# Kernel tuning notes

Hardware: AMD Instinct MI355X
Metric: run time of the kernel (lower is better)

## Reference

```python
import jax, jax.numpy as jnp
import numpy as np
from jax import lax

B, C, H, W = 16, 128, 128, 128
COUT, KH, KW, K, RED, TEMP = 128, 3, 3, 4, 4, 30.0
ATTN_CH = max(C // RED, 1)

def setup_inputs() -> dict:
    key = jax.random.key(0)
    ks = jax.random.split(key, 7)
    fan_out = COUT * KH * KW
    std = np.sqrt(2.0 / fan_out)  # kaiming_normal fan_out, relu
    return {
        "x": jax.random.normal(ks[0], (B, C, H, W), dtype=jnp.float32),
        "weight": jax.random.normal(ks[1], (K, COUT, C, KH, KW), dtype=jnp.float32) * std,
        "bias": jnp.zeros((K, COUT), dtype=jnp.float32),
        "aw1": jax.random.normal(ks[2], (ATTN_CH, C), dtype=jnp.float32) * (1.0 / np.sqrt(C)),
        "ab1": jnp.zeros((ATTN_CH,), dtype=jnp.float32),
        "aw2": jax.random.normal(ks[3], (K, ATTN_CH), dtype=jnp.float32) * (1.0 / np.sqrt(ATTN_CH)),
        "ab2": jnp.zeros((K,), dtype=jnp.float32),
    }

def reference(x, weight, bias, aw1, ab1, aw2, ab2):
    # Attention branch: global avg pool -> 1x1 conv -> relu -> 1x1 conv
    pooled = jnp.mean(x, axis=(2, 3))                       # (B, C)
    h = jax.nn.relu(pooled @ aw1.T + ab1)                   # (B, attn_ch)
    scores = h @ aw2.T + ab2                                # (B, K)
    attn = jax.nn.softmax(scores / TEMP, axis=1)            # (B, K)

    # Per-sample aggregated kernel and bias
    agg_w = jnp.einsum('bk,koipq->boipq', attn, weight)     # (B, Cout, Cin, kH, kW)
    agg_b = attn @ bias                                     # (B, Cout)

    # Per-sample conv2d (stride 1, padding 1, dilation 1, groups 1)
    def conv_one(xi, wi):
        return lax.conv_general_dilated(
            xi[None], wi,
            window_strides=(1, 1),
            padding=((1, 1), (1, 1)),
            dimension_numbers=('NCHW', 'OIHW', 'NCHW'),
        )[0]

    out = jax.vmap(conv_one)(x, agg_w)                      # (B, Cout, H, W)
    return out + agg_b[:, :, None, None]
```

## Files before the change

kernel.cpp:

```cpp
#include <hip/hip_runtime.h>

typedef float f32x4 __attribute__((ext_vector_type(4)));
typedef short bf16x8 __attribute__((ext_vector_type(8)));

__device__ __forceinline__ unsigned short f2bf(float f) {
  unsigned u = __builtin_bit_cast(unsigned, f);
  u = (u + 0x7FFFu + ((u >> 16) & 1u)) >> 16;
  return (unsigned short)u;
}

__device__ __forceinline__ void async16(const unsigned short* g, unsigned short* l) {
  __builtin_amdgcn_global_load_lds(
      (__attribute__((address_space(1))) void*)g,
      (__attribute__((address_space(3))) void*)l, 16, 0, 0);
}

#define XT_ROW 16640

__global__ __launch_bounds__(256) void k_transpose(const float* __restrict__ x,
                                                   unsigned short* __restrict__ xt,
                                                   float* __restrict__ rowsum) {
  __shared__ unsigned short tile[128][128];
  __shared__ float psum[128][8];
  const int y = blockIdx.x, b = blockIdx.y;
  const int t = threadIdx.x;
  const int colb = (t & 7) * 16;
  const int cp = t >> 3;
  const int swz = (t & 7) << 3;
  for (int ci = 0; ci < 4; ++ci) {
    const int c = ci * 32 + cp;
    const int c2 = c ^ swz;
    const float* src = x + (((size_t)(b * 128 + c) * 128 + y) * 128 + colb);
    float s = 0.f;
#pragma unroll
    for (int j = 0; j < 16; j += 4) {
      float4 v = *(const float4*)(src + j);
      s += v.x + v.y + v.z + v.w;
      tile[colb + j + 0][c2] = f2bf(v.x);
      tile[colb + j + 1][c2] = f2bf(v.y);
      tile[colb + j + 2][c2] = f2bf(v.z);
      tile[colb + j + 3][c2] = f2bf(v.w);
    }
    psum[c][t & 7] = s;
  }
  __syncthreads();
#pragma unroll
  for (int it = 0; it < 8; ++it) {
    const int slot = t + it * 256;
    const int col = slot >> 4;
    const int cg = (slot & 15) * 8;
    const int c2 = cg ^ (((col >> 4) & 7) << 3);
    uint4 vv = *(const uint4*)&tile[col][c2];
    *(uint4*)(xt + (((size_t)b * 130 + y + 1) * 130 + col + 1) * 128 + cg) = vv;
  }
  if (t < 128) {
    float r = 0.f;
#pragma unroll
    for (int j = 0; j < 8; ++j) r += psum[t][j];
    rowsum[((size_t)b * 128 + t) * 128 + y] = r;
  }
}

__global__ __launch_bounds__(256) void k_border(unsigned short* __restrict__ xt) {
  const int b = blockIdx.y;
  const int idx = blockIdx.x * 256 + threadIdx.x;
  if (idx >= 8256) return;
  int row, col, ck;
  if (idx < 4160) {
    row = (idx < 2080) ? 0 : 129;
    const int s = idx % 2080;
    col = s >> 4;
    ck = s & 15;
  } else {
    const int s = idx - 4160;
    row = (s >> 5) + 1;
    col = (s & 16) ? 129 : 0;
    ck = s & 15;
  }
  uint4 z = {0, 0, 0, 0};
  *(uint4*)(xt + ((size_t)b * 130 + row) * 130 * 128 + (size_t)col * 128 + ck * 8) = z;
}

__global__ __launch_bounds__(128) void k_attn(const float* __restrict__ rowsum,
                                              const float* __restrict__ aw1,
                                              const float* __restrict__ ab1,
                                              const float* __restrict__ aw2,
                                              const float* __restrict__ ab2,
                                              const float* __restrict__ bias,
                                              float* __restrict__ attn,
                                              float* __restrict__ aggb) {
  __shared__ float pooled[128];
  __shared__ float h[32];
  __shared__ float at[4];
  const int b = blockIdx.x, t = threadIdx.x;
  const float* rs = rowsum + (size_t)(b * 128 + t) * 128;
  float s = 0.f;
  for (int yy = 0; yy < 128; ++yy) s += rs[yy];
  pooled[t] = s * (1.f / 16384.f);
  __syncthreads();
  if (t < 32) {
    float hv = ab1[t];
    for (int c = 0; c < 128; ++c) hv += pooled[c] * aw1[t * 128 + c];
    h[t] = fmaxf(hv, 0.f);
  }
  __syncthreads();
  if (t < 4) {
    float sc = ab2[t];
    for (int a = 0; a < 32; ++a) sc += h[a] * aw2[t * 32 + a];
    at[t] = sc * (1.f / 30.f);
  }
  __syncthreads();
  if (t == 0) {
    float m = fmaxf(fmaxf(at[0], at[1]), fmaxf(at[2], at[3]));
    float e0 = __expf(at[0] - m), e1 = __expf(at[1] - m);
    float e2 = __expf(at[2] - m), e3 = __expf(at[3] - m);
    float inv = 1.f / (e0 + e1 + e2 + e3);
    at[0] = e0 * inv; at[1] = e1 * inv; at[2] = e2 * inv; at[3] = e3 * inv;
  }
  __syncthreads();
  if (t < 4) attn[b * 4 + t] = at[t];
  float ab = 0.f;
  for (int k = 0; k < 4; ++k) ab += at[k] * bias[k * 128 + t];
  aggb[b * 128 + t] = ab;
}

__global__ __launch_bounds__(256) void k_aggw(const float* __restrict__ weight,
                                              const float* __restrict__ attn,
                                              unsigned short* __restrict__ aggw) {
  const int fid = blockIdx.x * 256 + threadIdx.x;
  const int kk = fid & 31;
  const int o = (fid >> 5) & 127;
  const int rest = fid >> 12;
  const int s = rest % 36;
  const int b = rest / 36;
  const int c = ((s & 3) << 5) + kk;
  const int pq = s >> 2;
  const size_t src = (size_t)o * 1152 + (size_t)c * 9 + pq;
  float v = attn[b * 4 + 0] * weight[src]
          + attn[b * 4 + 1] * weight[src + 147456]
          + attn[b * 4 + 2] * weight[src + 2 * 147456]
          + attn[b * 4 + 3] * weight[src + 3 * 147456];
  aggw[fid] = f2bf(v);
}

__global__ __launch_bounds__(512, 1) void k_conv(const unsigned short* __restrict__ xt,
                                                 const unsigned short* __restrict__ aggw,
                                                 const float* __restrict__ aggb,
                                                 float* __restrict__ out) {
  __shared__ unsigned short lds[81920];
  const int id = blockIdx.x;
  const int swz = (id & 7) * 128 + (id >> 3);
  const int b = swz >> 6;
  const int y0 = (swz & 63) * 2;
  const int t = threadIdx.x;
  const int lane = t & 63, w = t >> 6;
  const int mw = w >> 2, nw = w & 3;
  const int l15 = lane & 15, lk = lane >> 4;

  {
    const unsigned short* xb = xt + (size_t)(b * 130 + y0) * XT_ROW;
#pragma unroll
    for (int i = 0; i < 16; ++i) {
      const int idx = i * 512 + t;
      const int row = idx >> 11, col = (idx >> 4) & 127, k8 = idx & 15;
      async16(xb + (row * 130 + col + 1) * 128 + ((k8 ^ (col & 15)) * 8),
              &lds[0] + i * 4096 + w * 512);
    }
  }
  const int an = t >> 2, ak8 = t & 3;
  const unsigned short* aS = aggw + (size_t)b * 147456 + an * 32
                           + ((ak8 ^ ((an >> 1) & 3)) * 8);
  unsigned short* aldsw = &lds[65536] + w * 512;

#define STAGE_A(buf, s) async16(aS + (s) * 4096, aldsw + (buf) * 4096)

  STAGE_A(0, 0);
  STAGE_A(1, 1);

  const int r_ = nw >> 1;
  const int px0 = (nw & 1) * 64 + l15;
  f32x4 acc[4][4] = {};

#pragma unroll
  for (int g = 0; g < 18; ++g) {
    asm volatile("s_waitcnt vmcnt(0)" ::: "memory");
    __builtin_amdgcn_sched_barrier(0);
    __builtin_amdgcn_s_barrier();
    __builtin_amdgcn_sched_barrier(0);
    if (g + 1 < 18) { STAGE_A((2 * g + 2) & 3, 2 * g + 2);
                      STAGE_A((2 * g + 3) & 3, 2 * g + 3); }
    __builtin_amdgcn_sched_barrier(0);
#pragma unroll
    for (int ss = 0; ss < 2; ++ss) {
      const int s = 2 * g + ss;
      const int tap = s >> 2, cc = s & 3;
      const int p = tap / 3, q = tap - 3 * p;
      const unsigned short* A0 = &lds[65536 + (s & 3) * 4096];
      bf16x8 af[4], bfr[4];
#pragma unroll
      for (int mi = 0; mi < 4; ++mi) {
        const int row = mw * 64 + mi * 16 + l15;
        af[mi] = *(const bf16x8*)(A0 + row * 32 + ((lk ^ ((row >> 1) & 3)) * 8));
      }
#pragma unroll
      for (int ni = 0; ni < 4; ++ni) {
        const int icol = px0 + ni * 16 + q - 1;
        int ccl = icol;
        if (q == 0 && ni == 0) ccl = (icol < 0) ? 0 : icol;
        if (q == 2 && ni == 3) ccl = (icol > 127) ? 127 : icol;
        bfr[ni] = *(const bf16x8*)(&lds[0] + ((r_ + p) * 128 + ccl) * 128
                                   + (((cc * 4 + lk) ^ (ccl & 15)) * 8));
        if (q == 0 && ni == 0) { if (icol < 0)   bfr[ni] = (bf16x8)0; }
        if (q == 2 && ni == 3) { if (icol > 127) bfr[ni] = (bf16x8)0; }
      }
      __builtin_amdgcn_s_setprio(1);
#pragma unroll
      for (int mi = 0; mi < 4; ++mi)
#pragma unroll
        for (int ni = 0; ni < 4; ++ni)
          acc[mi][ni] = __builtin_amdgcn_mfma_f32_16x16x32_bf16(af[mi], bfr[ni], acc[mi][ni], 0, 0, 0);
      __builtin_amdgcn_s_setprio(0);
    }
  }
#undef STAGE_A

  const int y = y0 + r_;
  const int colb = (nw & 1) * 64 + l15;
#pragma unroll
  for (int mi = 0; mi < 4; ++mi) {
    const int o = mw * 64 + mi * 16 + lk * 4;
#pragma unroll
    for (int rr = 0; rr < 4; ++rr) {
      const float bsv = aggb[b * 128 + o + rr];
      float* orow = out + ((size_t)(b * 128 + o + rr) * 128 + y) * 128 + colb;
      orow[0]  = acc[mi][0][rr] + bsv;
      orow[16] = acc[mi][1][rr] + bsv;
      orow[32] = acc[mi][2][rr] + bsv;
      orow[48] = acc[mi][3][rr] + bsv;
    }
  }
}

extern "C" void kernel_launch(void* const* d_in, const int* in_sizes, int n_in,
                              void* d_out, int out_size, void* d_ws, size_t ws_size,
                              hipStream_t stream) {
  const float* x      = (const float*)d_in[0];
  const float* weight = (const float*)d_in[1];
  const float* bias   = (const float*)d_in[2];
  const float* aw1    = (const float*)d_in[3];
  const float* ab1    = (const float*)d_in[4];
  const float* aw2    = (const float*)d_in[5];
  const float* ab2    = (const float*)d_in[6];
  float* out = (float*)d_out;

  char* ws = (char*)d_ws;
  unsigned short* xt   = (unsigned short*)ws;
  unsigned short* aggw = (unsigned short*)(ws + 69222400);
  float* rowsum        = (float*)(ws + 69222400 + 4718592);
  float* attn          = (float*)(ws + 69222400 + 4718592 + 1048576);
  float* aggb          = (float*)(ws + 69222400 + 4718592 + 1048576 + 256);

  hipLaunchKernelGGL(k_border, dim3(33, 16), dim3(256), 0, stream, xt);
  hipLaunchKernelGGL(k_transpose, dim3(128, 16), dim3(256), 0, stream, x, xt, rowsum);
  hipLaunchKernelGGL(k_attn, dim3(16), dim3(128), 0, stream,
                     rowsum, aw1, ab1, aw2, ab2, bias, attn, aggb);
  hipLaunchKernelGGL(k_aggw, dim3(9216), dim3(256), 0, stream, weight, attn, aggw);
  hipLaunchKernelGGL(k_conv, dim3(1024), dim3(512), 0, stream, xt, aggw, aggb, out);
}
```

Baseline: 155.8 us.

## Switch conv LDS tiles to k8-major layout, dropping XOR swizzle

```diff
diff --git a/kernel.cpp b/kernel.cpp
--- a/kernel.cpp
+++ b/kernel.cpp
@@ -128,12 +128,13 @@
                                               const float* __restrict__ attn,
                                               unsigned short* __restrict__ aggw) {
   const int fid = blockIdx.x * 256 + threadIdx.x;
-  const int kk = fid & 31;
-  const int o = (fid >> 5) & 127;
+  const int e = fid & 7;
+  const int o = (fid >> 3) & 127;
+  const int k8 = (fid >> 10) & 3;
   const int rest = fid >> 12;
   const int s = rest % 36;
   const int b = rest / 36;
-  const int c = ((s & 3) << 5) + kk;
+  const int c = ((s & 3) << 5) + k8 * 8 + e;
   const int pq = s >> 2;
   const size_t src = (size_t)o * 1152 + (size_t)c * 9 + pq;
   float v = attn[b * 4 + 0] * weight[src]
@@ -162,14 +163,12 @@
 #pragma unroll
     for (int i = 0; i < 16; ++i) {
       const int idx = i * 512 + t;
-      const int row = idx >> 11, col = (idx >> 4) & 127, k8 = idx & 15;
-      async16(xb + (row * 130 + col + 1) * 128 + ((k8 ^ (col & 15)) * 8),
-              &lds[0] + i * 4096 + w * 512);
-    }
-  }
-  const int an = t >> 2, ak8 = t & 3;
-  const unsigned short* aS = aggw + (size_t)b * 147456 + an * 32
-                           + ((ak8 ^ ((an >> 1) & 3)) * 8);
+      const int row = idx >> 11, k8 = (idx >> 7) & 15, col = idx & 127;
+      async16(xb + ((size_t)row * 130 + col + 1) * 128 + k8 * 8,
+              &lds[0] + (size_t)(i * 512 + w * 64) * 8);
+    }
+  }
+  const unsigned short* aS = aggw + (size_t)b * 147456 + t * 8;
   unsigned short* aldsw = &lds[65536] + w * 512;
 
 #define STAGE_A(buf, s) async16(aS + (s) * 4096, aldsw + (buf) * 4096)
@@ -179,6 +178,8 @@
 
   const int r_ = nw >> 1;
   const int px0 = (nw & 1) * 64 + l15;
+  const unsigned short* Bb = &lds[0] + r_ * 16384 + lk * 1024 + px0 * 8;
+  const unsigned short* Ab = &lds[65536] + (lk * 128 + mw * 64 + l15) * 8;
   f32x4 acc[4][4] = {};
 
 #pragma unroll
@@ -195,23 +196,22 @@
       const int s = 2 * g + ss;
       const int tap = s >> 2, cc = s & 3;
       const int p = tap / 3, q = tap - 3 * p;
-      const unsigned short* A0 = &lds[65536 + (s & 3) * 4096];
       bf16x8 af[4], bfr[4];
 #pragma unroll
-      for (int mi = 0; mi < 4; ++mi) {
-        const int row = mw * 64 + mi * 16 + l15;
-        af[mi] = *(const bf16x8*)(A0 + row * 32 + ((lk ^ ((row >> 1) & 3)) * 8));
-      }
+      for (int mi = 0; mi < 4; ++mi)
+        af[mi] = *(const bf16x8*)(Ab + (s & 3) * 4096 + mi * 128);
 #pragma unroll
       for (int ni = 0; ni < 4; ++ni) {
-        const int icol = px0 + ni * 16 + q - 1;
-        int ccl = icol;
-        if (q == 0 && ni == 0) ccl = (icol < 0) ? 0 : icol;
-        if (q == 2 && ni == 3) ccl = (icol > 127) ? 127 : icol;
-        bfr[ni] = *(const bf16x8*)(&lds[0] + ((r_ + p) * 128 + ccl) * 128
-                                   + (((cc * 4 + lk) ^ (ccl & 15)) * 8));
-        if (q == 0 && ni == 0) { if (icol < 0)   bfr[ni] = (bf16x8)0; }
-        if (q == 2 && ni == 3) { if (icol > 127) bfr[ni] = (bf16x8)0; }
+        if ((q == 0 && ni == 0) || (q == 2 && ni == 3)) {
+          const int icol = px0 + ni * 16 + q - 1;
+          const int ccl = icol < 0 ? 0 : (icol > 127 ? 127 : icol);
+          bfr[ni] = *(const bf16x8*)(&lds[0] + (r_ + p) * 16384
+                                     + (cc * 4 + lk) * 1024 + ccl * 8);
+          if (icol < 0 || icol > 127) bfr[ni] = (bf16x8)0;
+        } else {
+          bfr[ni] = *(const bf16x8*)(Bb + p * 16384 + cc * 4096
+                                     + (ni * 16 + q - 1) * 8);
+        }
       }
       __builtin_amdgcn_s_setprio(1);
 #pragma unroll
```

Result: slower. 163.7 us (+5.0%).
